# Kernel tuning notes

Hardware: AMD Instinct MI355X
Metric: run time of the kernel (lower is better)

Reference implementation:

```python
import jax, jax.numpy as jnp
import numpy as np

H, KVH, HD = 16, 8, 64
EPS = 1e-6
SCALING = HD ** -0.5


def _rms_norm(x, w):
    # RMSNorm over last dim (head_dim)
    var = jnp.mean(x * x, axis=-1, keepdims=True)
    return x * jax.lax.rsqrt(var + EPS) * w


def _rotate_half(x):
    x1, x2 = jnp.split(x, 2, axis=-1)
    return jnp.concatenate([-x2, x1], axis=-1)


def setup_inputs() -> dict:
    key = jax.random.key(0)
    ks = jax.random.split(key, 12)
    B, Q, CTX, HID = 1, 2048, 2048, 1024
    NB, T = 32, 64  # Q == NB * T
    TOTAL = CTX + Q
    inp = {}
    inp["hidden_states"] = jax.random.normal(ks[0], (B, Q, HID), jnp.float32)
    inp["target_hidden"] = jax.random.normal(ks[1], (B, CTX, HID), jnp.float32)
    pos = jnp.arange(TOTAL, dtype=jnp.float32)[:, None]
    inv = 1.0 / (10000.0 ** (jnp.arange(0, HD, 2, dtype=jnp.float32) / HD))
    ang = pos * inv[None, :]
    emb = jnp.concatenate([ang, ang], axis=-1)
    inp["cos"] = jnp.cos(emb)[None]  # [B, TOTAL, HD]
    inp["sin"] = jnp.sin(emb)[None]
    inp["attention_mask"] = jnp.zeros((B, 1, Q, TOTAL), jnp.float32)
    s = 0.02
    inp["Wq"] = jax.random.normal(ks[2], (HID, H * HD), jnp.float32) * s
    inp["Wk"] = jax.random.normal(ks[3], (HID, KVH * HD), jnp.float32) * s
    inp["Wv"] = jax.random.normal(ks[4], (HID, KVH * HD), jnp.float32) * s
    inp["Wo"] = jax.random.normal(ks[5], (H * HD, HID), jnp.float32) * s
    inp["q_norm_w"] = jnp.ones((HD,), jnp.float32)
    inp["k_norm_w"] = jnp.ones((HD,), jnp.float32)
    inp["tree_bias"] = jax.random.normal(ks[6], (64, H), jnp.float32) * s
    inp["relation_map"] = jax.random.randint(ks[7], (B, NB, T, T), 0, 64, jnp.int32)
    return inp


def reference(hidden_states, target_hidden, cos, sin, attention_mask,
              Wq, Wk, Wv, Wo, q_norm_w, k_norm_w, tree_bias, relation_map):
    B, Q, HID = hidden_states.shape
    CTX = target_hidden.shape[1]
    TOTAL = CTX + Q
    NB, T = relation_map.shape[1], relation_map.shape[2]
    groups = H // KVH

    q = (hidden_states @ Wq).reshape(B, Q, H, HD)
    k_ctx = target_hidden @ Wk
    k_noise = hidden_states @ Wk
    v_ctx = target_hidden @ Wv
    v_noise = hidden_states @ Wv
    k = jnp.concatenate([k_ctx, k_noise], axis=1).reshape(B, TOTAL, KVH, HD)
    v = jnp.concatenate([v_ctx, v_noise], axis=1).reshape(B, TOTAL, KVH, HD)

    q = _rms_norm(q, q_norm_w).transpose(0, 2, 1, 3)  # [B,H,Q,HD]
    k = _rms_norm(k, k_norm_w).transpose(0, 2, 1, 3)  # [B,KVH,TOTAL,HD]
    v = v.transpose(0, 2, 1, 3)

    cos_b = cos[:, None]  # [B,1,TOTAL,HD]
    sin_b = sin[:, None]
    q = q * cos_b[..., -Q:, :] + _rotate_half(q) * sin_b[..., -Q:, :]
    k = k * cos_b + _rotate_half(k) * sin_b

    # GQA: repeat kv heads
    k = jnp.repeat(k, groups, axis=1)  # [B,H,TOTAL,HD]
    v = jnp.repeat(v, groups, axis=1)

    scores = jnp.einsum('bhqd,bhkd->bhqk', q, k) * SCALING  # [B,H,Q,TOTAL]
    scores = scores + attention_mask

    # tree positional bias: block-diagonal (same tree) on the noise-noise block
    bias = tree_bias[relation_map]                 # [B,NB,T,T,H]
    bias = jnp.transpose(bias, (0, 4, 1, 2, 3))    # [B,H,NB,T,T]
    s_noise = scores[..., CTX:].reshape(B, H, NB, T, NB, T)
    idx = jnp.arange(NB)
    s_noise = s_noise.at[:, :, idx, :, idx, :].add(jnp.transpose(bias, (2, 0, 1, 3, 4)))
    scores = jnp.concatenate([scores[..., :CTX], s_noise.reshape(B, H, Q, Q)], axis=-1)

    attn = jax.nn.softmax(scores, axis=-1)
    out = jnp.einsum('bhqk,bhkd->bhqd', attn, v)   # [B,H,Q,HD]
    out = out.transpose(0, 2, 1, 3).reshape(B, Q, H * HD)
    return out @ Wo
```

## Files before the change

### kernel.cpp

```cpp
#include <hip/hip_runtime.h>
#include <hip/hip_bf16.h>

typedef __bf16 bf16x8 __attribute__((ext_vector_type(8)));
typedef float  f32x4  __attribute__((ext_vector_type(4)));

__device__ inline unsigned short f2bf(float f) {
    unsigned int u = __float_as_uint(f);
    u += 0x7fffu + ((u >> 16) & 1u);
    return (unsigned short)(u >> 16);
}
__device__ inline float bf2f(unsigned int s) {
    return __uint_as_float(s << 16);
}
__device__ inline unsigned int pk2bf(float a, float b) {
    __hip_bfloat162 h = __float22bfloat162_rn(make_float2(a, b));
    union { __hip_bfloat162 h; unsigned int u; } cv;
    cv.h = h;
    return cv.u;
}
__device__ inline f32x4 mfma16(bf16x8 a, bf16x8 b, f32x4 c) {
    return __builtin_amdgcn_mfma_f32_16x16x32_bf16(a, b, c, 0, 0, 0);
}
__device__ inline void gload_lds16(const void* g, void* l) {
    __builtin_amdgcn_global_load_lds(
        (const __attribute__((address_space(1))) void*)g,
        (__attribute__((address_space(3))) void*)l, 16, 0, 0);
}

__global__ __launch_bounds__(256) void prep1(const float* __restrict__ th, const float* __restrict__ hs,
                                             const float* __restrict__ Wk, const float* __restrict__ Wv,
                                             const float* __restrict__ Wq, const float* __restrict__ Wo,
                                             unsigned short* __restrict__ X,
                                             unsigned short* __restrict__ Wkvt,
                                             unsigned short* __restrict__ Wqt,
                                             unsigned short* __restrict__ Wot) {
    __shared__ float t[64][65];
    int bx = blockIdx.x, tid = threadIdx.x;
    if (bx < 4096) {
        int i = bx * 256 + tid;
        const int n4 = 2048 * 1024 / 4;
        float4 v = (i < n4) ? ((const float4*)th)[i] : ((const float4*)hs)[i - n4];
        ((uint2*)X)[i] = make_uint2(pk2bf(v.x, v.y), pk2bf(v.z, v.w));
        return;
    }
    int t4 = bx - 4096;
    const float* in; unsigned short* out; int in_rs, xt, yt;
    if (t4 < 256)      { in = Wq; out = Wqt; in_rs = 1024; xt = t4 & 15; yt = t4 >> 4; }
    else if (t4 < 512) { t4 -= 256; in = Wo; out = Wot; in_rs = 1024; xt = t4 & 15; yt = t4 >> 4; }
    else if (t4 < 640) { t4 -= 512; in = Wk; out = Wkvt; in_rs = 512; xt = t4 & 7; yt = t4 >> 3; }
    else               { t4 -= 640; in = Wv; out = Wkvt + (size_t)512 * 1024; in_rs = 512; xt = t4 & 7; yt = t4 >> 3; }
    int r0 = yt * 64, c0b = xt * 64;
    int rr = tid >> 4, c4 = (tid & 15) * 4;
#pragma unroll
    for (int i = 0; i < 4; i++) {
        int r = rr + 16 * i;
        float4 v = *(const float4*)&in[(size_t)(r0 + r) * in_rs + c0b + c4];
        t[c4][r] = v.x; t[c4 + 1][r] = v.y; t[c4 + 2][r] = v.z; t[c4 + 3][r] = v.w;
    }
    __syncthreads();
#pragma unroll
    for (int i = 0; i < 4; i++) {
        int cc = rr + 16 * i;
        *(uint2*)&out[(size_t)(c0b + cc) * 1024 + r0 + c4] =
            make_uint2(pk2bf(t[cc][c4], t[cc][c4 + 1]), pk2bf(t[cc][c4 + 2], t[cc][c4 + 3]));
    }
}

union GemmLds {
    struct { unsigned short A[2][128 * 64]; unsigned short B[2][64 * 64]; } s;
    unsigned short Ost[128 * 72];
};

template <bool FP32OUT>
__device__ __forceinline__ void gemm_bk64(const unsigned short* __restrict__ A,
                                          const unsigned short* __restrict__ Bt,
                                          int m0, int n0,
                                          unsigned short* __restrict__ dstBf, int dstStride,
                                          const float* __restrict__ nw,
                                          const float* __restrict__ cosb,
                                          const float* __restrict__ sinb,
                                          int posBase, float scale,
                                          float* __restrict__ dstF,
                                          GemmLds* u) {
    int tid = threadIdx.x, wave = tid >> 6, lane = tid & 63, quad = lane >> 4, l16 = lane & 15;
    f32x4 acc[2][4] = {};

    int drow = lane >> 3;
    int sch = ((lane & 7) ^ drow) * 8;
    const unsigned short* AgB = A + (size_t)(m0 + wave * 32 + drow) * 1024 + sch;
    const unsigned short* BgB = Bt + (size_t)(n0 + wave * 16 + drow) * 1024 + sch;

    auto dma = [&](int k0, int b) {
#pragma unroll
        for (int ii = 0; ii < 4; ii++)
            gload_lds16(AgB + (size_t)ii * 8 * 1024 + k0, &u->s.A[b][(wave * 32 + ii * 8) * 64]);
#pragma unroll
        for (int jj = 0; jj < 2; jj++)
            gload_lds16(BgB + (size_t)jj * 8 * 1024 + k0, &u->s.B[b][(wave * 16 + jj * 8) * 64]);
    };
    dma(0, 0);

    for (int kt = 0; kt < 16; kt++) {
        int b = kt & 1;
        __syncthreads();
        if (kt < 15) dma((kt + 1) * 64, b ^ 1);
#pragma unroll
        for (int kk = 0; kk < 2; kk++) {
            int co = ((kk * 4 + quad) ^ (l16 & 7)) * 8;
            bf16x8 af0 = *(const bf16x8*)&u->s.A[b][(wave * 32 + l16) * 64 + co];
            bf16x8 af1 = *(const bf16x8*)&u->s.A[b][(wave * 32 + 16 + l16) * 64 + co];
            bf16x8 bq[4];
#pragma unroll
            for (int ng = 0; ng < 4; ng++)
                bq[ng] = *(const bf16x8*)&u->s.B[b][(ng * 16 + l16) * 64 + co];
#pragma unroll
            for (int ng = 0; ng < 4; ng++) {
                acc[0][ng] = mfma16(af0, bq[ng], acc[0][ng]);
                acc[1][ng] = mfma16(af1, bq[ng], acc[1][ng]);
            }
        }
    }

    if constexpr (FP32OUT) {
#pragma unroll
        for (int i = 0; i < 2; i++)
#pragma unroll
            for (int j = 0; j < 4; j++) {
                int m = m0 + wave * 32 + i * 16 + quad * 4;
                int n = n0 + j * 16 + l16;
#pragma unroll
                for (int r = 0; r < 4; r++)
                    dstF[(size_t)(m + r) * 1024 + n] = acc[i][j][r];
            }
        return;
    }

    __syncthreads();
    unsigned short* Ost = u->Ost;
    int c0 = l16, c1 = 16 + l16, c2 = 32 + l16, c3 = 48 + l16;
    if (nw) {
        float w0 = nw[c0], w1 = nw[c1], w2 = nw[c2], w3 = nw[c3];
#pragma unroll
        for (int i = 0; i < 2; i++) {
            float s[4];
#pragma unroll
            for (int r = 0; r < 4; r++)
                s[r] = acc[i][0][r] * acc[i][0][r] + acc[i][1][r] * acc[i][1][r] +
                       acc[i][2][r] * acc[i][2][r] + acc[i][3][r] * acc[i][3][r];
#pragma unroll
            for (int m = 1; m <= 8; m <<= 1) {
#pragma unroll
                for (int r = 0; r < 4; r++) s[r] += __shfl_xor(s[r], m);
            }
#pragma unroll
            for (int r = 0; r < 4; r++) {
                float rn = rsqrtf(s[r] * (1.0f / 64.0f) + 1e-6f);
                int row = wave * 32 + i * 16 + quad * 4 + r;
                size_t pos = (size_t)(posBase + m0 + row) * 64;
                float x0 = acc[i][0][r] * rn * w0, x1 = acc[i][1][r] * rn * w1;
                float x2 = acc[i][2][r] * rn * w2, x3 = acc[i][3][r] * rn * w3;
                float y0 = fmaf(x0, cosb[pos + c0], -x2 * sinb[pos + c0]) * scale;
                float y1 = fmaf(x1, cosb[pos + c1], -x3 * sinb[pos + c1]) * scale;
                float y2 = fmaf(x2, cosb[pos + c2],  x0 * sinb[pos + c2]) * scale;
                float y3 = fmaf(x3, cosb[pos + c3],  x1 * sinb[pos + c3]) * scale;
                Ost[row * 72 + c0] = f2bf(y0);
                Ost[row * 72 + c1] = f2bf(y1);
                Ost[row * 72 + c2] = f2bf(y2);
                Ost[row * 72 + c3] = f2bf(y3);
            }
        }
    } else {
#pragma unroll
        for (int i = 0; i < 2; i++)
#pragma unroll
            for (int r = 0; r < 4; r++) {
                int row = wave * 32 + i * 16 + quad * 4 + r;
                Ost[row * 72 + c0] = f2bf(acc[i][0][r]);
                Ost[row * 72 + c1] = f2bf(acc[i][1][r]);
                Ost[row * 72 + c2] = f2bf(acc[i][2][r]);
                Ost[row * 72 + c3] = f2bf(acc[i][3][r]);
            }
    }
    __syncthreads();
    int row = tid >> 3, c = (tid & 7) * 8;
#pragma unroll
    for (int i = 0; i < 4; i++) {
        int rr = row + 32 * i;
        uint4 val = *(uint4*)&Ost[rr * 72 + c];
        *(uint4*)&dstBf[(size_t)(m0 + rr) * dstStride + c] = val;
    }
}

__global__ __launch_bounds__(256) void gemm_qkv(const unsigned short* __restrict__ X,
                                                const unsigned short* __restrict__ Wkvt,
                                                const unsigned short* __restrict__ Wqt,
                                                const float* __restrict__ qnw,
                                                const float* __restrict__ knw,
                                                const float* __restrict__ cosb,
                                                const float* __restrict__ sinb,
                                                unsigned short* __restrict__ Qb,
                                                unsigned short* __restrict__ Kb,
                                                unsigned short* __restrict__ Vraw) {
    __shared__ GemmLds u;
    int bx = blockIdx.x, ny = blockIdx.y;
    if (bx < 32) {
        if (ny < 8)
            gemm_bk64<false>(X, Wkvt, bx * 128, ny * 64,
                             Kb + (size_t)ny * 4096 * 64, 64, knw, cosb, sinb, 0, 1.0f, nullptr, &u);
        else
            gemm_bk64<false>(X, Wkvt, bx * 128, ny * 64,
                             Vraw + (ny - 8) * 64, 512, nullptr, nullptr, nullptr, 0, 1.0f, nullptr, &u);
    } else {
        gemm_bk64<false>(X + (size_t)2048 * 1024, Wqt, (bx - 32) * 128, ny * 64,
                         Qb + (size_t)ny * 2048 * 64, 64, qnw, cosb, sinb, 2048,
                         0.18033688011112042f, nullptr, &u);
    }
}

__global__ __launch_bounds__(256) void gemm_wo(const unsigned short* __restrict__ A,
                                               const unsigned short* __restrict__ Bt,
                                               float* __restrict__ C) {
    __shared__ GemmLds u;
    gemm_bk64<true>(A, Bt, blockIdx.x * 128, blockIdx.y * 64,
                    nullptr, 0, nullptr, nullptr, nullptr, 0, 1.0f, C, &u);
}

__global__ __launch_bounds__(256) void vtrans(const unsigned short* __restrict__ Vraw,
                                              unsigned short* __restrict__ Vtr) {
    __shared__ float t[64][65];
    int t4 = blockIdx.x;
    int xk = t4 & 63, z = t4 >> 6;
    const unsigned short* ip = Vraw + (size_t)xk * 64 * 512 + z * 64;
    unsigned short* op = Vtr + (size_t)z * 64 * 4096 + (size_t)xk * 64;
    int tid = threadIdx.x, rr = tid >> 4, c0 = (tid & 15) * 4;
#pragma unroll
    for (int i = 0; i < 4; i++) {
        int r = rr + 16 * i;
        uint2 v = *(const uint2*)&ip[(size_t)r * 512 + c0];
        t[c0][r]     = bf2f(v.x & 0xffff);
        t[c0 + 1][r] = bf2f(v.x >> 16);
        t[c0 + 2][r] = bf2f(v.y & 0xffff);
        t[c0 + 3][r] = bf2f(v.y >> 16);
    }
    __syncthreads();
#pragma unroll
    for (int i = 0; i < 4; i++) {
        int d = rr + 16 * i;
        *(uint2*)&op[(size_t)d * 4096 + c0] =
            make_uint2(pk2bf(t[d][c0], t[d][c0 + 1]), pk2bf(t[d][c0 + 2], t[d][c0 + 3]));
    }
}

__global__ __launch_bounds__(256) void attn7(const unsigned short* __restrict__ Qb,
                                             const unsigned short* __restrict__ Kb,
                                             const unsigned short* __restrict__ Vt,
                                             const int* __restrict__ relmap,
                                             const float* __restrict__ tree_bias,
                                             unsigned short* __restrict__ Opart,
                                             float* __restrict__ Lpart) {
    __shared__ alignas(16) union {
        struct { unsigned short K[2][4096]; unsigned short V[2][4096]; unsigned short P[4][2048]; } s;
        unsigned short O[128 * 72];
    } u;

    int qt = blockIdx.x, h = blockIdx.y, ks = blockIdx.z, kvh = h >> 1;
    int tid = threadIdx.x, wave = tid >> 6, lane = tid & 63, quad = lane >> 4, l16 = lane & 15;

    bf16x8 qf[2][2];
#pragma unroll
    for (int qg = 0; qg < 2; qg++) {
        int q = qt * 128 + wave * 32 + qg * 16 + l16;
        const unsigned short* qp = Qb + ((size_t)h * 2048 + q) * 64 + quad * 8;
        qf[qg][0] = *(const bf16x8*)qp;
        qf[qg][1] = *(const bf16x8*)(qp + 32);
    }
    f32x4 o[4][2] = {};
    f32x4 lacc[2] = {};
    union { unsigned short us[8]; bf16x8 v; } one_u;
#pragma unroll
    for (int i = 0; i < 8; i++) one_u.us[i] = 0x3F80;
    const bf16x8 ones = one_u.v;

    int drow = lane >> 3;
    int sch = ((lane & 7) ^ drow) * 8;
    const unsigned short* KgB = Kb + ((size_t)kvh * 4096 + ks * 1024) * 64;
    const unsigned short* VgB = Vt + (size_t)kvh * 64 * 4096 + ks * 1024;
    int r0 = wave * 16, r1 = r0 + 8;
    const unsigned short* Kg0 = KgB + (size_t)(r0 + drow) * 64 + sch;
    const unsigned short* Kg1 = KgB + (size_t)(r1 + drow) * 64 + sch;
    const unsigned short* Vg0 = VgB + (size_t)(r0 + drow) * 4096 + sch;
    const unsigned short* Vg1 = VgB + (size_t)(r1 + drow) * 4096 + sch;

    auto dma = [&](int kt, int b) {
        gload_lds16(Kg0 + kt * 4096, &u.s.K[b][r0 * 64]);
        gload_lds16(Kg1 + kt * 4096, &u.s.K[b][r1 * 64]);
        gload_lds16(Vg0 + kt * 64, &u.s.V[b][r0 * 64]);
        gload_lds16(Vg1 + kt * 64, &u.s.V[b][r1 * 64]);
    };
    dma(0, 0);

    unsigned short* pw = &u.s.P[wave][0];
    int sw = l16 & 7;
    int psw = (l16 & 7) * 2;
    int nb = 2 * qt + (wave >> 1);
    int bias_kt = 32 + nb - ks * 16;
    const float LOG2E = 1.4426950408889634f;

    for (int kt = 0; kt < 16; kt++) {
        int b = kt & 1;
        __syncthreads();
        if (kt + 1 < 16) dma(kt + 1, b ^ 1);

#pragma unroll
        for (int g = 0; g < 4; g++) {
            int krow = (g * 16 + l16) * 64;
            bf16x8 kf0 = *(const bf16x8*)&u.s.K[b][krow + ((quad ^ sw) * 8)];
            bf16x8 kf1 = *(const bf16x8*)&u.s.K[b][krow + (((4 + quad) ^ sw) * 8)];
            float pv[2][4];
#pragma unroll
            for (int qg = 0; qg < 2; qg++) {
                f32x4 s = {};
                s = mfma16(kf0, qf[qg][0], s);
                s = mfma16(kf1, qf[qg][1], s);
#pragma unroll
                for (int r = 0; r < 4; r++) pv[qg][r] = s[r];
            }
            if (kt == bias_kt) {
#pragma unroll
                for (int qg = 0; qg < 2; qg++)
#pragma unroll
                    for (int r = 0; r < 4; r++) {
                        int t1 = (wave & 1) * 32 + qg * 16 + l16;
                        int t2 = g * 16 + quad * 4 + r;
                        int rel = relmap[nb * 4096 + t1 * 64 + t2];
                        pv[qg][r] += tree_bias[rel * 16 + h] * LOG2E;
                    }
            }
#pragma unroll
            for (int qg = 0; qg < 2; qg++) {
                float p0 = __builtin_amdgcn_exp2f(pv[qg][0]);
                float p1 = __builtin_amdgcn_exp2f(pv[qg][1]);
                float p2 = __builtin_amdgcn_exp2f(pv[qg][2]);
                float p3 = __builtin_amdgcn_exp2f(pv[qg][3]);
                *(uint2*)&pw[(qg * 16 + l16) * 64 + (((g * 4 + quad) ^ psw) * 4)] =
                    make_uint2(pk2bf(p0, p1), pk2bf(p2, p3));
            }
        }
        bf16x8 pf[2][2];
#pragma unroll
        for (int qg = 0; qg < 2; qg++) {
            pf[qg][0] = *(const bf16x8*)&pw[(qg * 16 + l16) * 64 + (((quad * 2) ^ psw) * 4)];
            pf[qg][1] = *(const bf16x8*)&pw[(qg * 16 + l16) * 64 + (((8 + quad * 2) ^ psw) * 4)];
            lacc[qg] = mfma16(ones, pf[qg][0], lacc[qg]);
            lacc[qg] = mfma16(ones, pf[qg][1], lacc[qg]);
        }
#pragma unroll
        for (int dg = 0; dg < 4; dg++) {
            int vrow = (dg * 16 + l16) * 64;
            bf16x8 vf0 = *(const bf16x8*)&u.s.V[b][vrow + ((quad ^ sw) * 8)];
            bf16x8 vf1 = *(const bf16x8*)&u.s.V[b][vrow + (((4 + quad) ^ sw) * 8)];
#pragma unroll
            for (int qg = 0; qg < 2; qg++) {
                o[dg][qg] = mfma16(vf0, pf[qg][0], o[dg][qg]);
                o[dg][qg] = mfma16(vf1, pf[qg][1], o[dg][qg]);
            }
        }
    }
    __syncthreads();

    float lv0 = lacc[0][0], lv1 = lacc[1][0];
#pragma unroll
    for (int qg = 0; qg < 2; qg++) {
        int qlocal = wave * 32 + qg * 16 + l16;
#pragma unroll
        for (int dg = 0; dg < 4; dg++) {
            f32x4 ov = o[dg][qg];
            *(uint2*)&u.O[qlocal * 72 + dg * 16 + quad * 4] =
                make_uint2(pk2bf(ov[0], ov[1]), pk2bf(ov[2], ov[3]));
        }
        if (quad == 0)
            Lpart[((size_t)ks * 16 + h) * 2048 + qt * 128 + qlocal] = qg ? lv1 : lv0;
    }
    __syncthreads();
    int row = tid >> 3, c = (tid & 7) * 8;
#pragma unroll
    for (int i = 0; i < 4; i++) {
        int rr = row + 32 * i;
        uint4 val = *(uint4*)&u.O[rr * 72 + c];
        size_t q = qt * 128 + rr;
        *(uint4*)&Opart[((size_t)ks * 2048 + q) * 1024 + h * 64 + c] = val;
    }
}

__global__ __launch_bounds__(256) void combine4(const unsigned short* __restrict__ Op,
                                                const float* __restrict__ Lp,
                                                unsigned short* __restrict__ AO) {
    int t = blockIdx.x * 256 + threadIdx.x;
    int q = t >> 7, h = (t >> 3) & 15, c8 = (t & 7) * 8;
    size_t base = ((size_t)q * 16 + h) * 64 + c8;
    float s[8] = {};
    float l = 0.0f;
#pragma unroll
    for (int ks = 0; ks < 4; ks++) {
        uint4 v = *(const uint4*)&Op[(size_t)ks * 2097152 + base];
        s[0] += bf2f(v.x & 0xffff); s[1] += bf2f(v.x >> 16);
        s[2] += bf2f(v.y & 0xffff); s[3] += bf2f(v.y >> 16);
        s[4] += bf2f(v.z & 0xffff); s[5] += bf2f(v.z >> 16);
        s[6] += bf2f(v.w & 0xffff); s[7] += bf2f(v.w >> 16);
        l += Lp[((size_t)ks * 16 + h) * 2048 + q];
    }
    float inv = 1.0f / l;
    uint4 r;
    r.x = pk2bf(s[0] * inv, s[1] * inv);
    r.y = pk2bf(s[2] * inv, s[3] * inv);
    r.z = pk2bf(s[4] * inv, s[5] * inv);
    r.w = pk2bf(s[6] * inv, s[7] * inv);
    *(uint4*)&AO[base] = r;
}

extern "C" void kernel_launch(void* const* d_in, const int* in_sizes, int n_in,
                              void* d_out, int out_size, void* d_ws, size_t ws_size,
                              hipStream_t stream) {
    const float* hs   = (const float*)d_in[0];
    const float* th   = (const float*)d_in[1];
    const float* cosb = (const float*)d_in[2];
    const float* sinb = (const float*)d_in[3];
    const float* Wq  = (const float*)d_in[5];
    const float* Wk  = (const float*)d_in[6];
    const float* Wv  = (const float*)d_in[7];
    const float* Wo  = (const float*)d_in[8];
    const float* qnw = (const float*)d_in[9];
    const float* knw = (const float*)d_in[10];
    const float* tb  = (const float*)d_in[11];
    const int*   rm  = (const int*)d_in[12];
    float* out = (float*)d_out;

    char* ws = (char*)d_ws;
    size_t off = 0;
    auto alloc = [&](size_t b) { char* p = ws + off; off += (b + 255) & ~(size_t)255; return p; };
    char*           pool  = alloc((size_t)16 * 1024 * 1024);
    unsigned short* X     = (unsigned short*)pool;
    unsigned short* Vraw  = (unsigned short*)(pool + (size_t)8 * 1024 * 1024);
    unsigned short* Opart = (unsigned short*)pool;
    unsigned short* Wqt   = (unsigned short*)alloc((size_t)1024 * 1024 * 2);
    unsigned short* Wkvt  = (unsigned short*)alloc((size_t)1024 * 1024 * 2);
    unsigned short* Wot   = (unsigned short*)alloc((size_t)1024 * 1024 * 2);
    unsigned short* Qb    = (unsigned short*)alloc((size_t)16 * 2048 * 64 * 2);
    unsigned short* Kb    = (unsigned short*)alloc((size_t)8 * 4096 * 64 * 2);
    unsigned short* Vtr   = (unsigned short*)alloc((size_t)8 * 64 * 4096 * 2);
    unsigned short* AOb   = (unsigned short*)alloc((size_t)2048 * 1024 * 2);
    float*          Lpart = (float*)alloc((size_t)4 * 16 * 2048 * 4);

    prep1<<<4864, 256, 0, stream>>>(th, hs, Wk, Wv, Wq, Wo, X, Wkvt, Wqt, Wot);
    gemm_qkv<<<dim3(48, 16), 256, 0, stream>>>(X, Wkvt, Wqt, qnw, knw, cosb, sinb, Qb, Kb, Vraw);
    vtrans<<<512, 256, 0, stream>>>(Vraw, Vtr);
    attn7<<<dim3(16, 16, 4), 256, 0, stream>>>(Qb, Kb, Vtr, rm, tb, Opart, Lpart);
    combine4<<<1024, 256, 0, stream>>>(Opart, Lpart, AOb);
    gemm_wo<<<dim3(16, 16), 256, 0, stream>>>(AOb, Wot, out);
}
```

Before: 204.9 us.

## Split attention P tile into two halves and use 64-row tiles for Wo GEMM

The attention kernel now computes scores, exp and PV in two 32-key halves per K tile. This halves the per-wave P scratch in LDS (2048 to 1024 elements) and lets the PV MFMAs start earlier, with a new XOR swizzle for the narrower P rows. The output projection gets a dedicated 64x64-tile GEMM launched on a 32x16 grid, doubling the block count to improve CU occupancy on the small 2048x1024 problem. The trade-off is less register reuse per block in the Wo GEMM and a possible shift in the interleaving of LDS traffic and MFMAs in attention.

```diff
diff --git a/kernel.cpp b/kernel.cpp
--- a/kernel.cpp
+++ b/kernel.cpp
@@ -71,7 +71,6 @@
     unsigned short Ost[128 * 72];
 };
 
-template <bool FP32OUT>
 __device__ __forceinline__ void gemm_bk64(const unsigned short* __restrict__ A,
                                           const unsigned short* __restrict__ Bt,
                                           int m0, int n0,
@@ -80,7 +79,6 @@
                                           const float* __restrict__ cosb,
                                           const float* __restrict__ sinb,
                                           int posBase, float scale,
-                                          float* __restrict__ dstF,
                                           GemmLds* u) {
     int tid = threadIdx.x, wave = tid >> 6, lane = tid & 63, quad = lane >> 4, l16 = lane & 15;
     f32x4 acc[2][4] = {};
@@ -119,20 +117,6 @@
                 acc[1][ng] = mfma16(af1, bq[ng], acc[1][ng]);
             }
         }
-    }
-
-    if constexpr (FP32OUT) {
-#pragma unroll
-        for (int i = 0; i < 2; i++)
-#pragma unroll
-            for (int j = 0; j < 4; j++) {
-                int m = m0 + wave * 32 + i * 16 + quad * 4;
-                int n = n0 + j * 16 + l16;
-#pragma unroll
-                for (int r = 0; r < 4; r++)
-                    dstF[(size_t)(m + r) * 1024 + n] = acc[i][j][r];
-            }
-        return;
     }
 
     __syncthreads();
@@ -205,24 +189,61 @@
     int bx = blockIdx.x, ny = blockIdx.y;
     if (bx < 32) {
         if (ny < 8)
-            gemm_bk64<false>(X, Wkvt, bx * 128, ny * 64,
-                             Kb + (size_t)ny * 4096 * 64, 64, knw, cosb, sinb, 0, 1.0f, nullptr, &u);
+            gemm_bk64(X, Wkvt, bx * 128, ny * 64,
+                      Kb + (size_t)ny * 4096 * 64, 64, knw, cosb, sinb, 0, 1.0f, &u);
         else
-            gemm_bk64<false>(X, Wkvt, bx * 128, ny * 64,
-                             Vraw + (ny - 8) * 64, 512, nullptr, nullptr, nullptr, 0, 1.0f, nullptr, &u);
+            gemm_bk64(X, Wkvt, bx * 128, ny * 64,
+                      Vraw + (ny - 8) * 64, 512, nullptr, nullptr, nullptr, 0, 1.0f, &u);
     } else {
-        gemm_bk64<false>(X + (size_t)2048 * 1024, Wqt, (bx - 32) * 128, ny * 64,
-                         Qb + (size_t)ny * 2048 * 64, 64, qnw, cosb, sinb, 2048,
-                         0.18033688011112042f, nullptr, &u);
-    }
-}
-
-__global__ __launch_bounds__(256) void gemm_wo(const unsigned short* __restrict__ A,
-                                               const unsigned short* __restrict__ Bt,
-                                               float* __restrict__ C) {
-    __shared__ GemmLds u;
-    gemm_bk64<true>(A, Bt, blockIdx.x * 128, blockIdx.y * 64,
-                    nullptr, 0, nullptr, nullptr, nullptr, 0, 1.0f, C, &u);
+        gemm_bk64(X + (size_t)2048 * 1024, Wqt, (bx - 32) * 128, ny * 64,
+                  Qb + (size_t)ny * 2048 * 64, 64, qnw, cosb, sinb, 2048,
+                  0.18033688011112042f, &u);
+    }
+}
+
+__global__ __launch_bounds__(256) void gemm_wo64(const unsigned short* __restrict__ A,
+                                                 const unsigned short* __restrict__ Bt,
+                                                 float* __restrict__ C) {
+    __shared__ struct { unsigned short A[2][4096]; unsigned short B[2][4096]; } u;
+    int m0 = blockIdx.x * 64, n0 = blockIdx.y * 64;
+    int tid = threadIdx.x, wave = tid >> 6, lane = tid & 63, quad = lane >> 4, l16 = lane & 15;
+    f32x4 acc[4] = {};
+
+    int drow = lane >> 3;
+    int sch = ((lane & 7) ^ drow) * 8;
+    const unsigned short* Ag0 = A + (size_t)(m0 + wave * 16 + drow) * 1024 + sch;
+    const unsigned short* Bg0 = Bt + (size_t)(n0 + wave * 16 + drow) * 1024 + sch;
+
+    auto dma = [&](int k0, int b) {
+        gload_lds16(Ag0 + k0, &u.A[b][(wave * 16) * 64]);
+        gload_lds16(Ag0 + (size_t)8 * 1024 + k0, &u.A[b][(wave * 16 + 8) * 64]);
+        gload_lds16(Bg0 + k0, &u.B[b][(wave * 16) * 64]);
+        gload_lds16(Bg0 + (size_t)8 * 1024 + k0, &u.B[b][(wave * 16 + 8) * 64]);
+    };
+    dma(0, 0);
+
+    for (int kt = 0; kt < 16; kt++) {
+        int b = kt & 1;
+        __syncthreads();
+        if (kt < 15) dma((kt + 1) * 64, b ^ 1);
+#pragma unroll
+        for (int kk = 0; kk < 2; kk++) {
+            int co = ((kk * 4 + quad) ^ (l16 & 7)) * 8;
+            bf16x8 af = *(const bf16x8*)&u.A[b][(wave * 16 + l16) * 64 + co];
+#pragma unroll
+            for (int ng = 0; ng < 4; ng++) {
+                bf16x8 bq = *(const bf16x8*)&u.B[b][(ng * 16 + l16) * 64 + co];
+                acc[ng] = mfma16(af, bq, acc[ng]);
+            }
+        }
+    }
+#pragma unroll
+    for (int j = 0; j < 4; j++) {
+        int n = n0 + j * 16 + l16;
+#pragma unroll
+        for (int r = 0; r < 4; r++)
+            C[(size_t)(m0 + wave * 16 + quad * 4 + r) * 1024 + n] = acc[j][r];
+    }
 }
 
 __global__ __launch_bounds__(256) void vtrans(const unsigned short* __restrict__ Vraw,
@@ -251,7 +272,7 @@
     }
 }
 
-__global__ __launch_bounds__(256) void attn7(const unsigned short* __restrict__ Qb,
+__global__ __launch_bounds__(256) void attn8(const unsigned short* __restrict__ Qb,
                                              const unsigned short* __restrict__ Kb,
                                              const unsigned short* __restrict__ Vt,
                                              const int* __restrict__ relmap,
@@ -259,7 +280,7 @@
                                              unsigned short* __restrict__ Opart,
                                              float* __restrict__ Lpart) {
     __shared__ alignas(16) union {
-        struct { unsigned short K[2][4096]; unsigned short V[2][4096]; unsigned short P[4][2048]; } s;
+        struct { unsigned short K[2][4096]; unsigned short V[2][4096]; unsigned short P[4][1024]; } s;
         unsigned short O[128 * 72];
     } u;
 
@@ -301,7 +322,7 @@
 
     unsigned short* pw = &u.s.P[wave][0];
     int sw = l16 & 7;
-    int psw = (l16 & 7) * 2;
+    int pxor = l16 & 6;
     int nb = 2 * qt + (wave >> 1);
     int bias_kt = 32 + nb - ks * 16;
     const float LOG2E = 1.4426950408889634f;
@@ -312,57 +333,60 @@
         if (kt + 1 < 16) dma(kt + 1, b ^ 1);
 
 #pragma unroll
-        for (int g = 0; g < 4; g++) {
-            int krow = (g * 16 + l16) * 64;
-            bf16x8 kf0 = *(const bf16x8*)&u.s.K[b][krow + ((quad ^ sw) * 8)];
-            bf16x8 kf1 = *(const bf16x8*)&u.s.K[b][krow + (((4 + quad) ^ sw) * 8)];
-            float pv[2][4];
+        for (int half = 0; half < 2; half++) {
+            float pv[2][2][4];
+#pragma unroll
+            for (int gl = 0; gl < 2; gl++) {
+                int g = half * 2 + gl;
+                int krow = (g * 16 + l16) * 64;
+                bf16x8 kf0 = *(const bf16x8*)&u.s.K[b][krow + ((quad ^ sw) * 8)];
+                bf16x8 kf1 = *(const bf16x8*)&u.s.K[b][krow + (((4 + quad) ^ sw) * 8)];
+#pragma unroll
+                for (int qg = 0; qg < 2; qg++) {
+                    f32x4 s = {};
+                    s = mfma16(kf0, qf[qg][0], s);
+                    s = mfma16(kf1, qf[qg][1], s);
+#pragma unroll
+                    for (int r = 0; r < 4; r++) pv[gl][qg][r] = s[r];
+                }
+            }
+            if (kt == bias_kt) {
+#pragma unroll
+                for (int gl = 0; gl < 2; gl++)
+#pragma unroll
+                    for (int qg = 0; qg < 2; qg++)
+#pragma unroll
+                        for (int r = 0; r < 4; r++) {
+                            int t1 = (wave & 1) * 32 + qg * 16 + l16;
+                            int t2 = (half * 2 + gl) * 16 + quad * 4 + r;
+                            int rel = relmap[nb * 4096 + t1 * 64 + t2];
+                            pv[gl][qg][r] += tree_bias[rel * 16 + h] * LOG2E;
+                        }
+            }
+#pragma unroll
+            for (int gl = 0; gl < 2; gl++)
+#pragma unroll
+                for (int qg = 0; qg < 2; qg++) {
+                    float p0 = __builtin_amdgcn_exp2f(pv[gl][qg][0]);
+                    float p1 = __builtin_amdgcn_exp2f(pv[gl][qg][1]);
+                    float p2 = __builtin_amdgcn_exp2f(pv[gl][qg][2]);
+                    float p3 = __builtin_amdgcn_exp2f(pv[gl][qg][3]);
+                    *(uint2*)&pw[(qg * 16 + l16) * 32 + (((gl * 4 + quad) ^ pxor) * 4)] =
+                        make_uint2(pk2bf(p0, p1), pk2bf(p2, p3));
+                }
+            bf16x8 pf[2];
 #pragma unroll
             for (int qg = 0; qg < 2; qg++) {
-                f32x4 s = {};
-                s = mfma16(kf0, qf[qg][0], s);
-                s = mfma16(kf1, qf[qg][1], s);
-#pragma unroll
-                for (int r = 0; r < 4; r++) pv[qg][r] = s[r];
-            }
-            if (kt == bias_kt) {
+                pf[qg] = *(const bf16x8*)&pw[(qg * 16 + l16) * 32 + (((quad * 2) ^ pxor) * 4)];
+                lacc[qg] = mfma16(ones, pf[qg], lacc[qg]);
+            }
+#pragma unroll
+            for (int dg = 0; dg < 4; dg++) {
+                int vrow = (dg * 16 + l16) * 64;
+                bf16x8 vf = *(const bf16x8*)&u.s.V[b][vrow + (((half * 4 + quad) ^ sw) * 8)];
 #pragma unroll
                 for (int qg = 0; qg < 2; qg++)
-#pragma unroll
-                    for (int r = 0; r < 4; r++) {
-                        int t1 = (wave & 1) * 32 + qg * 16 + l16;
-                        int t2 = g * 16 + quad * 4 + r;
-                        int rel = relmap[nb * 4096 + t1 * 64 + t2];
-                        pv[qg][r] += tree_bias[rel * 16 + h] * LOG2E;
-                    }
-            }
-#pragma unroll
-            for (int qg = 0; qg < 2; qg++) {
-                float p0 = __builtin_amdgcn_exp2f(pv[qg][0]);
-                float p1 = __builtin_amdgcn_exp2f(pv[qg][1]);
-                float p2 = __builtin_amdgcn_exp2f(pv[qg][2]);
-                float p3 = __builtin_amdgcn_exp2f(pv[qg][3]);
-                *(uint2*)&pw[(qg * 16 + l16) * 64 + (((g * 4 + quad) ^ psw) * 4)] =
-                    make_uint2(pk2bf(p0, p1), pk2bf(p2, p3));
-            }
-        }
-        bf16x8 pf[2][2];
-#pragma unroll
-        for (int qg = 0; qg < 2; qg++) {
-            pf[qg][0] = *(const bf16x8*)&pw[(qg * 16 + l16) * 64 + (((quad * 2) ^ psw) * 4)];
-            pf[qg][1] = *(const bf16x8*)&pw[(qg * 16 + l16) * 64 + (((8 + quad * 2) ^ psw) * 4)];
-            lacc[qg] = mfma16(ones, pf[qg][0], lacc[qg]);
-            lacc[qg] = mfma16(ones, pf[qg][1], lacc[qg]);
-        }
-#pragma unroll
-        for (int dg = 0; dg < 4; dg++) {
-            int vrow = (dg * 16 + l16) * 64;
-            bf16x8 vf0 = *(const bf16x8*)&u.s.V[b][vrow + ((quad ^ sw) * 8)];
-            bf16x8 vf1 = *(const bf16x8*)&u.s.V[b][vrow + (((4 + quad) ^ sw) * 8)];
-#pragma unroll
-            for (int qg = 0; qg < 2; qg++) {
-                o[dg][qg] = mfma16(vf0, pf[qg][0], o[dg][qg]);
-                o[dg][qg] = mfma16(vf1, pf[qg][1], o[dg][qg]);
+                    o[dg][qg] = mfma16(vf, pf[qg], o[dg][qg]);
             }
         }
     }
@@ -454,7 +478,7 @@
     prep1<<<4864, 256, 0, stream>>>(th, hs, Wk, Wv, Wq, Wo, X, Wkvt, Wqt, Wot);
     gemm_qkv<<<dim3(48, 16), 256, 0, stream>>>(X, Wkvt, Wqt, qnw, knw, cosb, sinb, Qb, Kb, Vraw);
     vtrans<<<512, 256, 0, stream>>>(Vraw, Vtr);
-    attn7<<<dim3(16, 16, 4), 256, 0, stream>>>(Qb, Kb, Vtr, rm, tb, Opart, Lpart);
+    attn8<<<dim3(16, 16, 4), 256, 0, stream>>>(Qb, Kb, Vtr, rm, tb, Opart, Lpart);
     combine4<<<1024, 256, 0, stream>>>(Opart, Lpart, AOb);
-    gemm_wo<<<dim3(16, 16), 256, 0, stream>>>(AOb, Wot, out);
-}
+    gemm_wo64<<<dim3(32, 16), 256, 0, stream>>>(AOb, Wot, out);
+}
```

Result: no change. 206.4 us (+0.8%).
